# Performance work log

Measured on AMD Instinct MI355X. Metric: run time of the kernel, lower is better.

## Reference

```python
import jax, jax.numpy as jnp
import numpy as np

NUM_HEADS = 8
SPLIT_S = 4
DIM = 288            # n_feat * 3 * 3
SCALE = (DIM // NUM_HEADS) ** -0.5  # quirk: uses full dim's head_dim (36), not reduced
EPS = 1e-5


def _extract_patches(x):
    # x: [B,C,H,W] -> [B, C*9, H*W], 3x3 kernel, stride 1, 'same' padding
    B, C, H, W = x.shape
    xp = jnp.pad(x, ((0, 0), (0, 0), (1, 1), (1, 1)))
    pats = jnp.stack([xp[:, :, i:i + H, j:j + W] for i in range(3) for j in range(3)], axis=2)
    return pats.reshape(B, C * 9, H * W)


def _fold(cols, H, W):
    # inverse of extract: [B, C*9, H*W] -> [B,C,H,W], summing overlapping patches
    B, Ck, _ = cols.shape
    C = Ck // 9
    p = cols.reshape(B, C, 3, 3, H, W)
    out = jnp.zeros((B, C, H + 2, W + 2), cols.dtype)
    for i in range(3):
        for j in range(3):
            out = out.at[:, :, i:i + H, j:j + W].add(p[:, :, i, j])
    return out[:, :, 1:H + 1, 1:W + 1]


def _ln(x, w, b):
    mu = x.mean(-1, keepdims=True)
    var = ((x - mu) ** 2).mean(-1, keepdims=True)
    return (x - mu) * jax.lax.rsqrt(var + EPS) * w + b


def _attn(x, reduce_w, qkv_w, proj_w, proj_b):
    # x: [B,N,288] -> reduce -> [B,N,144] -> block-diag attention over s=4 chunks
    x = x @ reduce_w.T
    B, N, C = x.shape
    hd = C // NUM_HEADS
    qkv = (x @ qkv_w.T).reshape(B, N, 3, NUM_HEADS, hd).transpose(2, 0, 3, 1, 4)
    q, k, v = qkv[0], qkv[1], qkv[2]          # [B,h,N,hd]
    chunk = N // SPLIT_S
    q = q.reshape(B, NUM_HEADS, SPLIT_S, chunk, hd)
    k = k.reshape(B, NUM_HEADS, SPLIT_S, chunk, hd)
    v = v.reshape(B, NUM_HEADS, SPLIT_S, chunk, hd)
    attn = jnp.einsum('bhscd,bhsed->bhsce', q, k) * SCALE   # [B,h,s,chunk,chunk]
    attn = jax.nn.softmax(attn, axis=-1)
    out = jnp.einsum('bhsce,bhsed->bhscd', attn, v)          # [B,h,s,chunk,hd]
    out = out.transpose(0, 2, 3, 1, 4).reshape(B, N, C)      # cat chunks on token dim
    return out @ proj_w.T + proj_b


def setup_inputs() -> dict:
    key = jax.random.key(0)
    ks = jax.random.split(key, 12)
    d, dr, dh = DIM, DIM // 2, DIM // 4  # 288, 144, 72
    f = lambda k, shape: (jax.random.normal(k, shape, jnp.float32) * 0.02)
    return {
        'x': jax.random.normal(ks[0], (4, 32, 64, 64), jnp.float32),
        'ln1_w': jnp.ones((d,), jnp.float32), 'ln1_b': jnp.zeros((d,), jnp.float32),
        'reduce_w': f(ks[1], (dr, d)),
        'qkv_w': f(ks[2], (3 * dr, dr)),
        'proj_w': f(ks[3], (d, dr)), 'proj_b': jnp.zeros((d,), jnp.float32),
        'ln2_w': jnp.ones((d,), jnp.float32), 'ln2_b': jnp.zeros((d,), jnp.float32),
        'fc1_w': f(ks[4], (dh, d)), 'fc1_b': jnp.zeros((dh,), jnp.float32),
        'fc2_w': f(ks[5], (d, dh)), 'fc2_b': jnp.zeros((d,), jnp.float32),
    }


def reference(x, ln1_w, ln1_b, reduce_w, qkv_w, proj_w, proj_b, ln2_w, ln2_b, fc1_w, fc1_b, fc2_w, fc2_b):
    B, C, H, W = x.shape
    t = _extract_patches(x).transpose(0, 2, 1)  # [B, N=H*W, 288]
    t = t + _attn(_ln(t, ln1_w, ln1_b), reduce_w, qkv_w, proj_w, proj_b)
    h = _ln(t, ln2_w, ln2_b)
    t = t + (jax.nn.relu(h @ fc1_w.T + fc1_b) @ fc2_w.T + fc2_b)
    return _fold(t.transpose(0, 2, 1), H, W)
```

## Files before the change

### kernel.cpp

```cpp
#include <hip/hip_runtime.h>
#include <hip/hip_bf16.h>

typedef __hip_bfloat16 bf16;
typedef unsigned short u16;
typedef unsigned int u32;
typedef __attribute__((ext_vector_type(8))) short bf16x8;
typedef __attribute__((ext_vector_type(4))) float f32x4;

#define BB 4
#define CCH 32
#define HH 64
#define WW 64
#define NN 4096
#define D 288
#define DR 144
#define DQ 432
#define NH 8
#define HD 18
#define SPLIT 4
#define CHUNK 1024
#define KS 512
#define DH 72
#define SCALE_ 0.16666666666666666f
#define QSCALE 0.24044917348149343f
#define EPS_ 1e-5f
#define ASTR 160
#define ATS 168
#define HSTR 96

__device__ __attribute__((aligned(16))) u16 g_Wcb[DQ * D];
__device__ __attribute__((aligned(16))) u16 g_pw[D * ASTR];
__device__ __attribute__((aligned(16))) u16 g_f1w[HSTR * D];
__device__ __attribute__((aligned(16))) u16 g_f2w[D * HSTR];
__device__ __attribute__((aligned(16))) u16 g_q[(size_t)BB * NH * NN * 32];
__device__ __attribute__((aligned(16))) u16 g_k[(size_t)BB * NH * NN * 32];
__device__ __attribute__((aligned(16))) u16 g_vt[(size_t)BB * NH * SPLIT * 32 * CHUNK];
__device__ __attribute__((aligned(16))) float g_part[2 * (size_t)BB * NH * NN * 20];
__device__ __attribute__((aligned(16))) u16 g_t0[(size_t)BB * NN * D];
__device__ __attribute__((aligned(16))) u16 g_t2b[(size_t)BB * D * NN];
__device__ int   g_flag;

__device__ __forceinline__ float b2f(bf16 v) { return __bfloat162float(v); }
__device__ __forceinline__ float bits2f(u16 u) { return __uint_as_float(((u32)u) << 16); }
__device__ __forceinline__ u16 f2bits(float f) {
    u32 u = __float_as_uint(f);
    return (u16)((u + 0x7FFF + ((u >> 16) & 1)) >> 16);
}
__device__ __forceinline__ float ldin(const void* p, size_t i, int isbf) {
    return isbf ? b2f(((const bf16*)p)[i]) : ((const float*)p)[i];
}

#define RS  (D * ASTR + HSTR * D + D * HSTR)
#define RS2 (RS + BB * NH * SPLIT * CHUNK)
#define RSB ((RS2 + 255) / 256)
#define PATCHB (BB * HH)

__global__ void k_prep(const void* __restrict__ x, const void* __restrict__ qkv_w,
                       const void* __restrict__ reduce_w, const void* __restrict__ proj_w,
                       const void* __restrict__ fc1_w, const void* __restrict__ fc2_w) {
    __shared__ int cnt4[4];
    __shared__ float qw[DR];
    __shared__ float slab[32 * 3 * 66];
    int tid = threadIdx.x;
    {
        const u16* u = (const u16*)x;
        int c = 0;
        for (int i = tid; i < 2048; i += 256) c += (((u[i] >> 7) & 0xFF) >= 0x90);
        for (int o = 32; o; o >>= 1) c += __shfl_xor(c, o);
        if ((tid & 63) == 0) cnt4[tid >> 6] = c;
    }
    __syncthreads();
    int bf = (cnt4[0] + cnt4[1] + cnt4[2] + cnt4[3]) < 32;
    if (tid == 0 && blockIdx.x == 0) g_flag = bf;

    int bid = blockIdx.x;
    if (bid < DQ) {
        int o = bid;
        if (tid < DR) qw[tid] = ldin(qkv_w, (size_t)o * DR + tid, bf);
        __syncthreads();
        for (int col = tid; col < D; col += 256) {
            float s0 = 0.f, s1 = 0.f;
            #pragma unroll 4
            for (int j = 0; j < DR; j += 2) {
                s0 += qw[j] * ldin(reduce_w, (size_t)j * D + col, bf);
                s1 += qw[j + 1] * ldin(reduce_w, (size_t)(j + 1) * D + col, bf);
            }
            g_Wcb[(size_t)o * D + col] = f2bits(s0 + s1);
        }
    } else if (bid < DQ + RSB) {
        int idx = (bid - DQ) * 256 + tid;
        if (idx < D * ASTR) {
            int o = idx / ASTR, j = idx % ASTR;
            g_pw[idx] = (j < DR) ? f2bits(ldin(proj_w, (size_t)o * DR + j, bf)) : (u16)0;
        } else if (idx < D * ASTR + HSTR * D) {
            int t = idx - D * ASTR;
            int o = t / D;
            g_f1w[t] = (o < DH) ? f2bits(ldin(fc1_w, (size_t)t, bf)) : (u16)0;
        } else if (idx < RS) {
            int t = idx - D * ASTR - HSTR * D;
            int o = t / HSTR, j = t % HSTR;
            g_f2w[t] = (j < DH) ? f2bits(ldin(fc2_w, (size_t)o * DH + j, bf)) : (u16)0;
        } else if (idx < RS2) {
            int t = idx - RS;
            int bhs = t >> 10, n = t & 1023;
            g_vt[((size_t)bhs * 32 + 18) * CHUNK + n] = 0x3F80;
        }
    } else {
        int pb = bid - DQ - RSB;
        int b = pb >> 6, y = pb & 63;
        for (int idx = tid; idx < 32 * 3 * 66; idx += 256) {
            int c = idx / 198, rem = idx % 198;
            int ki = rem / 66, col = rem % 66 - 1;
            int sy = y + ki - 1;
            float v = 0.f;
            if (col >= 0 && col < 64 && sy >= 0 && sy < 64)
                v = ldin(x, ((size_t)(b * CCH + c) * HH + sy) * WW + col, bf);
            slab[idx] = v;
        }
        __syncthreads();
        size_t obase = ((size_t)b * NN + y * 64) * D;
        for (int idx = tid; idx < 64 * D; idx += 256) {
            int t = idx / D, f = idx % D;
            int c = f / 9, k = f % 9, ki = k / 3, kj = k % 3;
            g_t0[obase + idx] = f2bits(slab[c * 198 + ki * 66 + t + kj]);
        }
    }
}

__global__ void k_ln_qkv(const void* __restrict__ lnw, const void* __restrict__ lnb) {
    __shared__ __attribute__((aligned(16))) u16 xln[32 * 296];
    __shared__ float lnwf[D], lnbf[D];
    __shared__ float smu[32], srs[32];
    __shared__ u16 buf[3][144][32];
    int bf = g_flag;
    int tid = threadIdx.x;
    size_t tok0 = (size_t)blockIdx.x * 32;
    for (int i = tid; i < D; i += 256) { lnwf[i] = ldin(lnw, i, bf); lnbf[i] = ldin(lnb, i, bf); }
    {
        int tt = tid >> 3, p = tid & 7;
        const u32* pr = (const u32*)(g_t0 + (tok0 + tt) * D + p * 36);
        float s = 0.f, q = 0.f;
        #pragma unroll
        for (int j = 0; j < 18; ++j) {
            u32 v = pr[j];
            float a = bits2f((u16)(v & 0xFFFF)), b = bits2f((u16)(v >> 16));
            s += a + b; q += a * a + b * b;
        }
        #pragma unroll
        for (int o = 1; o < 8; o <<= 1) { s += __shfl_xor(s, o); q += __shfl_xor(q, o); }
        if (p == 0) {
            float mu = s / D;
            smu[tt] = mu;
            srs[tt] = rsqrtf(q / D - mu * mu + EPS_);
        }
    }
    __syncthreads();
    for (int idx = tid; idx < 32 * 144; idx += 256) {
        int t = idx / 144, dw = idx % 144;
        u32 v = *(const u32*)(g_t0 + (tok0 + t) * D + 2 * dw);
        float mu = smu[t], rs = srs[t];
        int f = 2 * dw;
        float a = (bits2f((u16)(v & 0xFFFF)) - mu) * rs * lnwf[f] + lnbf[f];
        float b = (bits2f((u16)(v >> 16)) - mu) * rs * lnwf[f + 1] + lnbf[f + 1];
        *(u32*)&xln[t * 296 + f] = (u32)f2bits(a) | ((u32)f2bits(b) << 16);
    }
    __syncthreads();
    int w = tid >> 6, lane = tid & 63, quad = lane >> 4, l15 = lane & 15;
    bf16x8 areg0[9], areg1[9];
    {
        const u16* a0 = xln + l15 * 296 + quad * 8;
        const u16* a1 = xln + (16 + l15) * 296 + quad * 8;
        #pragma unroll
        for (int ks = 0; ks < 9; ++ks) {
            areg0[ks] = *(const bf16x8*)(a0 + ks * 32);
            areg1[ks] = *(const bf16x8*)(a1 + ks * 32);
        }
    }
    int nt0 = w * 7, nt1 = (nt0 + 7 > 27) ? 27 : nt0 + 7;
    for (int nt = nt0; nt < nt1; ++nt) {
        f32x4 acc0 = {0.f, 0.f, 0.f, 0.f}, acc1 = {0.f, 0.f, 0.f, 0.f};
        const u16* bbase = g_Wcb + (size_t)(nt * 16 + l15) * D + quad * 8;
        #pragma unroll
        for (int ks = 0; ks < 9; ++ks) {
            bf16x8 bfr = *(const bf16x8*)(bbase + ks * 32);
            acc0 = __builtin_amdgcn_mfma_f32_16x16x32_bf16(areg0[ks], bfr, acc0, 0, 0, 0);
            acc1 = __builtin_amdgcn_mfma_f32_16x16x32_bf16(areg1[ks], bfr, acc1, 0, 0, 0);
        }
        int o = nt * 16 + l15;
        int which = o / DR, rem = o % DR;
        #pragma unroll
        for (int r = 0; r < 4; ++r) {
            buf[which][rem][quad * 4 + r] = f2bits(which == 0 ? acc0[r] * QSCALE : acc0[r]);
            buf[which][rem][16 + quad * 4 + r] = f2bits(which == 0 ? acc1[r] * QSCALE : acc1[r]);
        }
    }
    __syncthreads();
    {
        int b_ = (int)(tok0 >> 12);
        int n0 = (int)(tok0 & 4095);
        int sIdx = n0 >> 10, nc = n0 & 1023;
        for (int idx = tid; idx < 2 * 8 * 32 * 9; idx += 256) {
            int which = idx / 2304;
            int r2 = idx - which * 2304;
            int h = r2 / 288, r3 = r2 % 288, t = r3 / 9, dw = r3 % 9;
            u32 lo = buf[which][h * 18 + 2 * dw][t];
            u32 hi = buf[which][h * 18 + 2 * dw + 1][t];
            u16* dst = (which ? g_k : g_q) + ((size_t)(b_ * NH + h) * NN + n0 + t) * 32 + 2 * dw;
            *(u32*)dst = lo | (hi << 16);
        }
        for (int idx = tid; idx < 144 * 16; idx += 256) {
            int rem = idx >> 4, tp = idx & 15;
            int hh = rem / HD, dd = rem % HD;
            u32 lo = buf[2][rem][2 * tp];
            u32 hi = buf[2][rem][2 * tp + 1];
            size_t voff = (((size_t)(b_ * NH + hh) * SPLIT + sIdx) * 32 + dd) * CHUNK + nc + 2 * tp;
            *(u32*)&g_vt[voff] = lo | (hi << 16);
        }
    }
}

#define PSTR 72
__global__ __launch_bounds__(128) void k_attn() {
    __shared__ __attribute__((aligned(16))) u16 Pl[2][4][16 * PSTR];
    int bid = blockIdx.x;
    int chunk = bid & 127;
    int qblk = (bid >> 7) & 7;
    int ksl = bid >> 10;
    int s = chunk & 3, bh = chunk >> 2;
    int tid = threadIdx.x;
    int w = tid >> 6, lane = tid & 63, quad = lane >> 4, l15 = lane & 15;

    size_t rowbase = (size_t)bh * NN + s * CHUNK;
    size_t vtbase = ((size_t)bh * SPLIT + s) * 32 * CHUNK;
    const u16* kbase = g_k + rowbase * 32 + quad * 8;
    const u16* vbase = g_vt + vtbase + quad * 8;

    int qbase = qblk * 128 + w * 64;
    bf16x8 qf[4];
    #pragma unroll
    for (int t = 0; t < 4; ++t)
        qf[t] = *(const bf16x8*)(g_q + (rowbase + qbase + t * 16 + l15) * 32 + quad * 8);

    f32x4 accA[4], accB[4];
    #pragma unroll
    for (int t = 0; t < 4; ++t) {
        accA[t] = (f32x4){0.f, 0.f, 0.f, 0.f};
        accB[t] = (f32x4){0.f, 0.f, 0.f, 0.f};
    }

    int kt0 = ksl * KS;
    for (int kk = 0; kk < KS; kk += 64) {
        int kt = kt0 + kk;
        bf16x8 kf0 = *(const bf16x8*)(kbase + (size_t)(kt + 2 * l15) * 32);
        bf16x8 kf1 = *(const bf16x8*)(kbase + (size_t)(kt + 2 * l15 + 1) * 32);
        bf16x8 kf2 = *(const bf16x8*)(kbase + (size_t)(kt + 32 + 2 * l15) * 32);
        bf16x8 kf3 = *(const bf16x8*)(kbase + (size_t)(kt + 33 + 2 * l15) * 32);
        bf16x8 vA0 = *(const bf16x8*)(vbase + (size_t)l15 * CHUNK + kt);
        bf16x8 vB0 = *(const bf16x8*)(vbase + (size_t)(16 + l15) * CHUNK + kt);
        bf16x8 vA1 = *(const bf16x8*)(vbase + (size_t)l15 * CHUNK + kt + 32);
        bf16x8 vB1 = *(const bf16x8*)(vbase + (size_t)(16 + l15) * CHUNK + kt + 32);
        f32x4 z = {0.f, 0.f, 0.f, 0.f};
        #pragma unroll
        for (int t = 0; t < 4; ++t) {
            u16* pw = Pl[w][t];
            f32x4 S0 = __builtin_amdgcn_mfma_f32_16x16x32_bf16(qf[t], kf0, z, 0, 0, 0);
            f32x4 S1 = __builtin_amdgcn_mfma_f32_16x16x32_bf16(qf[t], kf1, z, 0, 0, 0);
            f32x4 S2 = __builtin_amdgcn_mfma_f32_16x16x32_bf16(qf[t], kf2, z, 0, 0, 0);
            f32x4 S3 = __builtin_amdgcn_mfma_f32_16x16x32_bf16(qf[t], kf3, z, 0, 0, 0);
            #pragma unroll
            for (int r = 0; r < 4; ++r) {
                float p0 = exp2f(S0[r]), p1 = exp2f(S1[r]);
                float p2 = exp2f(S2[r]), p3 = exp2f(S3[r]);
                u32 w0 = __builtin_amdgcn_perm(__float_as_uint(p1), __float_as_uint(p0), 0x07060302u);
                u32 w1 = __builtin_amdgcn_perm(__float_as_uint(p3), __float_as_uint(p2), 0x07060302u);
                *(u32*)&pw[(quad * 4 + r) * PSTR + 2 * l15] = w0;
                *(u32*)&pw[(quad * 4 + r) * PSTR + 32 + 2 * l15] = w1;
            }
        }
        #pragma unroll
        for (int t = 0; t < 4; ++t) {
            const u16* pw = Pl[w][t];
            bf16x8 pf0 = *(const bf16x8*)&pw[l15 * PSTR + quad * 8];
            bf16x8 pf1 = *(const bf16x8*)&pw[l15 * PSTR + 32 + quad * 8];
            accA[t] = __builtin_amdgcn_mfma_f32_16x16x32_bf16(pf0, vA0, accA[t], 0, 0, 0);
            accB[t] = __builtin_amdgcn_mfma_f32_16x16x32_bf16(pf0, vB0, accB[t], 0, 0, 0);
            accA[t] = __builtin_amdgcn_mfma_f32_16x16x32_bf16(pf1, vA1, accA[t], 0, 0, 0);
            accB[t] = __builtin_amdgcn_mfma_f32_16x16x32_bf16(pf1, vB1, accB[t], 0, 0, 0);
        }
    }
    float* pb = g_part + (((size_t)ksl * 32 + bh) * SPLIT + s) * (size_t)(CHUNK * 20);
    #pragma unroll
    for (int t = 0; t < 4; ++t) {
        #pragma unroll
        for (int r = 0; r < 4; ++r) {
            int tokenc = qbase + t * 16 + quad * 4 + r;
            float* row = pb + (size_t)tokenc * 20;
            row[l15] = accA[t][r];
            if (l15 < 3) row[16 + l15] = accB[t][r];
        }
    }
}

__global__ void k_proj_mlp(const void* __restrict__ proj_b, const void* __restrict__ lnw,
                           const void* __restrict__ lnb, const void* __restrict__ fc1_b,
                           const void* __restrict__ fc2_b) {
    __shared__ __attribute__((aligned(16))) u16 t1f[32 * 296];
    __shared__ __attribute__((aligned(16))) u16 xln[32 * 296];
    __shared__ __attribute__((aligned(16))) u16 attnT[32 * ATS];
    __shared__ __attribute__((aligned(16))) u16 hbuf[32 * HSTR];
    __shared__ float lnwf[D], lnbf[D];
    __shared__ float smu[32], srs[32];
    int bf = g_flag;
    int tid = threadIdx.x;
    size_t tok0 = (size_t)blockIdx.x * 32;
    int w = tid >> 6, lane = tid & 63, quad = lane >> 4, l15 = lane & 15;
    for (int i = tid; i < D; i += 256) { lnwf[i] = ldin(lnw, i, bf); lnbf[i] = ldin(lnb, i, bf); }

    int b_ = (int)(tok0 >> 12);
    int s_ = ((int)tok0 & 4095) >> 10;
    int tc0 = (int)tok0 & 1023;
    for (int idx = tid; idx < 32 * (ATS - DR); idx += 256) {
        int t = idx / (ATS - DR), f = idx % (ATS - DR);
        attnT[t * ATS + DR + f] = 0;
    }
    {
        int t = tid >> 3, h = tid & 7;
        const float* p1 = g_part + (((size_t)(b_ * NH + h)) * SPLIT + s_) * (size_t)(CHUNK * 20)
                        + (size_t)(tc0 + t) * 20;
        const float* p2 = p1 + (size_t)32 * SPLIT * CHUNK * 20;
        f32x4 a0 = *(const f32x4*)p1,        c0 = *(const f32x4*)p2;
        f32x4 a1 = *(const f32x4*)(p1 + 4),  c1 = *(const f32x4*)(p2 + 4);
        f32x4 a2 = *(const f32x4*)(p1 + 8),  c2 = *(const f32x4*)(p2 + 8);
        f32x4 a3 = *(const f32x4*)(p1 + 12), c3 = *(const f32x4*)(p2 + 12);
        f32x4 a4 = *(const f32x4*)(p1 + 16), c4 = *(const f32x4*)(p2 + 16);
        float inv = 1.f / (a4[2] + c4[2]);
        u16* dst = attnT + t * ATS + h * HD;
        #pragma unroll
        for (int d = 0; d < 4; ++d) {
            dst[d]      = f2bits((a0[d] + c0[d]) * inv);
            dst[4 + d]  = f2bits((a1[d] + c1[d]) * inv);
            dst[8 + d]  = f2bits((a2[d] + c2[d]) * inv);
            dst[12 + d] = f2bits((a3[d] + c3[d]) * inv);
        }
        dst[16] = f2bits((a4[0] + c4[0]) * inv);
        dst[17] = f2bits((a4[1] + c4[1]) * inv);
    }
    __syncthreads();

    {
        bf16x8 areg0[5], areg1[5];
        const u16* a0 = attnT + l15 * ATS + quad * 8;
        const u16* a1 = attnT + (16 + l15) * ATS + quad * 8;
        #pragma unroll
        for (int ks = 0; ks < 5; ++ks) {
            areg0[ks] = *(const bf16x8*)(a0 + ks * 32);
            areg1[ks] = *(const bf16x8*)(a1 + ks * 32);
        }
        const int tab[5] = {0, 5, 10, 14, 18};
        for (int nt = tab[w]; nt < tab[w + 1]; ++nt) {
            f32x4 acc0 = {0.f, 0.f, 0.f, 0.f}, acc1 = {0.f, 0.f, 0.f, 0.f};
            const u16* bbase = g_pw + (size_t)(nt * 16 + l15) * ASTR + quad * 8;
            #pragma unroll
            for (int ks = 0; ks < 5; ++ks) {
                bf16x8 bfr = *(const bf16x8*)(bbase + ks * 32);
                acc0 = __builtin_amdgcn_mfma_f32_16x16x32_bf16(areg0[ks], bfr, acc0, 0, 0, 0);
                acc1 = __builtin_amdgcn_mfma_f32_16x16x32_bf16(areg1[ks], bfr, acc1, 0, 0, 0);
            }
            int o = nt * 16 + l15;
            float bias = ldin(proj_b, o, bf);
            #pragma unroll
            for (int r = 0; r < 4; ++r) {
                t1f[(quad * 4 + r) * 296 + o] =
                    f2bits(bits2f(g_t0[(tok0 + quad * 4 + r) * D + o]) + acc0[r] + bias);
                t1f[(16 + quad * 4 + r) * 296 + o] =
                    f2bits(bits2f(g_t0[(tok0 + 16 + quad * 4 + r) * D + o]) + acc1[r] + bias);
            }
        }
    }
    __syncthreads();
    {
        int tt = tid >> 3, p = tid & 7;
        const u32* src = (const u32*)&t1f[tt * 296 + p * 36];
        float s = 0.f, q = 0.f;
        #pragma unroll
        for (int j = 0; j < 18; ++j) {
            u32 v = src[j];
            float a = bits2f((u16)(v & 0xFFFF)), b = bits2f((u16)(v >> 16));
            s += a + b; q += a * a + b * b;
        }
        #pragma unroll
        for (int o = 1; o < 8; o <<= 1) { s += __shfl_xor(s, o); q += __shfl_xor(q, o); }
        if (p == 0) {
            float mu = s / D;
            smu[tt] = mu;
            srs[tt] = rsqrtf(q / D - mu * mu + EPS_);
        }
    }
    __syncthreads();
    for (int idx = tid; idx < 32 * 144; idx += 256) {
        int t = idx / 144, dw = idx % 144;
        int f = 2 * dw;
        u32 v = *(const u32*)&t1f[t * 296 + f];
        float mu = smu[t], rs = srs[t];
        float a = (bits2f((u16)(v & 0xFFFF)) - mu) * rs * lnwf[f] + lnbf[f];
        float b = (bits2f((u16)(v >> 16)) - mu) * rs * lnwf[f + 1] + lnbf[f + 1];
        *(u32*)&xln[t * 296 + f] = (u32)f2bits(a) | ((u32)f2bits(b) << 16);
    }
    __syncthreads();
    {
        bf16x8 areg0[9], areg1[9];
        const u16* a0 = xln + l15 * 296 + quad * 8;
        const u16* a1 = xln + (16 + l15) * 296 + quad * 8;
        #pragma unroll
        for (int ks = 0; ks < 9; ++ks) {
            areg0[ks] = *(const bf16x8*)(a0 + ks * 32);
            areg1[ks] = *(const bf16x8*)(a1 + ks * 32);
        }
        const int tab2[5] = {0, 2, 4, 5, 6};
        for (int nt = tab2[w]; nt < tab2[w + 1]; ++nt) {
            f32x4 acc0 = {0.f, 0.f, 0.f, 0.f}, acc1 = {0.f, 0.f, 0.f, 0.f};
            const u16* bbase = g_f1w + (size_t)(nt * 16 + l15) * D + quad * 8;
            #pragma unroll
            for (int ks = 0; ks < 9; ++ks) {
                bf16x8 bfr = *(const bf16x8*)(bbase + ks * 32);
                acc0 = __builtin_amdgcn_mfma_f32_16x16x32_bf16(areg0[ks], bfr, acc0, 0, 0, 0);
                acc1 = __builtin_amdgcn_mfma_f32_16x16x32_bf16(areg1[ks], bfr, acc1, 0, 0, 0);
            }
            int o = nt * 16 + l15;
            float bias = (o < DH) ? ldin(fc1_b, o, bf) : 0.f;
            #pragma unroll
            for (int r = 0; r < 4; ++r) {
                hbuf[(quad * 4 + r) * HSTR + o] = f2bits(fmaxf(acc0[r] + bias, 0.f));
                hbuf[(16 + quad * 4 + r) * HSTR + o] = f2bits(fmaxf(acc1[r] + bias, 0.f));
            }
        }
    }
    __syncthreads();
    {
        bf16x8 areg0[3], areg1[3];
        const u16* a0 = hbuf + l15 * HSTR + quad * 8;
        const u16* a1 = hbuf + (16 + l15) * HSTR + quad * 8;
        #pragma unroll
        for (int ks = 0; ks < 3; ++ks) {
            areg0[ks] = *(const bf16x8*)(a0 + ks * 32);
            areg1[ks] = *(const bf16x8*)(a1 + ks * 32);
        }
        const int tab[5] = {0, 5, 10, 14, 18};
        for (int nt = tab[w]; nt < tab[w + 1]; ++nt) {
            f32x4 acc0 = {0.f, 0.f, 0.f, 0.f}, acc1 = {0.f, 0.f, 0.f, 0.f};
            const u16* bbase = g_f2w + (size_t)(nt * 16 + l15) * HSTR + quad * 8;
            #pragma unroll
            for (int ks = 0; ks < 3; ++ks) {
                bf16x8 bfr = *(const bf16x8*)(bbase + ks * 32);
                acc0 = __builtin_amdgcn_mfma_f32_16x16x32_bf16(areg0[ks], bfr, acc0, 0, 0, 0);
                acc1 = __builtin_amdgcn_mfma_f32_16x16x32_bf16(areg1[ks], bfr, acc1, 0, 0, 0);
            }
            int o = nt * 16 + l15;
            float bias = ldin(fc2_b, o, bf);
            #pragma unroll
            for (int r = 0; r < 4; ++r) {
                xln[(quad * 4 + r) * 296 + o] =
                    f2bits(bits2f(t1f[(quad * 4 + r) * 296 + o]) + acc0[r] + bias);
                xln[(16 + quad * 4 + r) * 296 + o] =
                    f2bits(bits2f(t1f[(16 + quad * 4 + r) * 296 + o]) + acc1[r] + bias);
            }
        }
    }
    __syncthreads();
    {
        int n0 = (int)(tok0 & 4095);
        for (int idx = tid; idx < D * 16; idx += 256) {
            int o = idx >> 4, tp = idx & 15;
            u32 v = (u32)xln[(2 * tp) * 296 + o] | ((u32)xln[(2 * tp + 1) * 296 + o] << 16);
            *(u32*)&g_t2b[((size_t)b_ * D + o) * NN + n0 + 2 * tp] = v;
        }
    }
}

__global__ void k_fold(void* __restrict__ out) {
    int bf = g_flag;
    int idx = blockIdx.x * blockDim.x + threadIdx.x;
    if (idx >= BB * CCH * HH * WW) return;
    int xx = idx % WW;
    int y = (idx / WW) % HH;
    int c = (idx / (WW * HH)) % CCH;
    int b = idx / (WW * HH * CCH);
    const u16* base = g_t2b + ((size_t)b * D + c * 9) * NN;
    float s = 0.f;
    #pragma unroll
    for (int i = 0; i < 3; ++i) {
        int sy = y + 1 - i;
        if (sy < 0 || sy >= HH) continue;
        #pragma unroll
        for (int j = 0; j < 3; ++j) {
            int sx = xx + 1 - j;
            if (sx < 0 || sx >= WW) continue;
            s += bits2f(base[(size_t)(i * 3 + j) * NN + sy * WW + sx]);
        }
    }
    if (bf) ((bf16*)out)[idx] = __float2bfloat16(s);
    else    ((float*)out)[idx] = s;
}

extern "C" void kernel_launch(void* const* d_in, const int* in_sizes, int n_in,
                              void* d_out, int out_size, void* d_ws, size_t ws_size,
                              hipStream_t stream) {
    const void* x        = d_in[0];
    const void* ln1_w    = d_in[1];
    const void* ln1_b    = d_in[2];
    const void* reduce_w = d_in[3];
    const void* qkv_w    = d_in[4];
    const void* proj_w   = d_in[5];
    const void* proj_b   = d_in[6];
    const void* ln2_w    = d_in[7];
    const void* ln2_b    = d_in[8];
    const void* fc1_w    = d_in[9];
    const void* fc1_b    = d_in[10];
    const void* fc2_w    = d_in[11];
    const void* fc2_b    = d_in[12];

    k_prep     <<<DQ + RSB + PATCHB, 256, 0, stream>>>(x, qkv_w, reduce_w, proj_w, fc1_w, fc2_w);
    k_ln_qkv   <<<BB * NN / 32, 256, 0, stream>>>(ln1_w, ln1_b);
    k_attn     <<<2 * BB * NH * SPLIT * 8, 128, 0, stream>>>();
    k_proj_mlp <<<BB * NN / 32, 256, 0, stream>>>(proj_b, ln2_w, ln2_b, fc1_b, fc2_b);
    k_fold     <<<(BB * CCH * HH * WW + 255) / 256, 256, 0, stream>>>(d_out);
}
```

Baseline: 198.3 us.

## Fuse patch extraction into LN+QKV kernel and store attention partials in bf16

Patch extraction (im2col) moves out of the prep kernel into the LN/QKV kernel. Each 32-token block builds its own input slab in shared memory, and LayerNorm reads from there instead of re-reading g_t0 from global memory; g_t0 is still written for the later residual. The split-K attention partial outputs are now stored as bf16, with only the softmax denominator kept as fp32, which halves partial-buffer traffic at some cost in precision. The shared QKV output buffer is reused as the slab, which adds an extra barrier.

```diff
diff --git a/kernel.cpp b/kernel.cpp
--- a/kernel.cpp
+++ b/kernel.cpp
@@ -27,6 +27,7 @@
 #define ASTR 160
 #define ATS 168
 #define HSTR 96
+#define PROW 20
 
 __device__ __attribute__((aligned(16))) u16 g_Wcb[DQ * D];
 __device__ __attribute__((aligned(16))) u16 g_pw[D * ASTR];
@@ -35,7 +36,7 @@
 __device__ __attribute__((aligned(16))) u16 g_q[(size_t)BB * NH * NN * 32];
 __device__ __attribute__((aligned(16))) u16 g_k[(size_t)BB * NH * NN * 32];
 __device__ __attribute__((aligned(16))) u16 g_vt[(size_t)BB * NH * SPLIT * 32 * CHUNK];
-__device__ __attribute__((aligned(16))) float g_part[2 * (size_t)BB * NH * NN * 20];
+__device__ __attribute__((aligned(16))) u16 g_part[2 * (size_t)BB * NH * NN * PROW];
 __device__ __attribute__((aligned(16))) u16 g_t0[(size_t)BB * NN * D];
 __device__ __attribute__((aligned(16))) u16 g_t2b[(size_t)BB * D * NN];
 __device__ int   g_flag;
@@ -53,14 +54,12 @@
 #define RS  (D * ASTR + HSTR * D + D * HSTR)
 #define RS2 (RS + BB * NH * SPLIT * CHUNK)
 #define RSB ((RS2 + 255) / 256)
-#define PATCHB (BB * HH)
 
 __global__ void k_prep(const void* __restrict__ x, const void* __restrict__ qkv_w,
                        const void* __restrict__ reduce_w, const void* __restrict__ proj_w,
                        const void* __restrict__ fc1_w, const void* __restrict__ fc2_w) {
     __shared__ int cnt4[4];
     __shared__ float qw[DR];
-    __shared__ float slab[32 * 3 * 66];
     int tid = threadIdx.x;
     {
         const u16* u = (const u16*)x;
@@ -87,7 +86,7 @@
             }
             g_Wcb[(size_t)o * D + col] = f2bits(s0 + s1);
         }
-    } else if (bid < DQ + RSB) {
+    } else {
         int idx = (bid - DQ) * 256 + tid;
         if (idx < D * ASTR) {
             int o = idx / ASTR, j = idx % ASTR;
@@ -105,40 +104,44 @@
             int bhs = t >> 10, n = t & 1023;
             g_vt[((size_t)bhs * 32 + 18) * CHUNK + n] = 0x3F80;
         }
-    } else {
-        int pb = bid - DQ - RSB;
-        int b = pb >> 6, y = pb & 63;
-        for (int idx = tid; idx < 32 * 3 * 66; idx += 256) {
-            int c = idx / 198, rem = idx % 198;
-            int ki = rem / 66, col = rem % 66 - 1;
-            int sy = y + ki - 1;
-            float v = 0.f;
-            if (col >= 0 && col < 64 && sy >= 0 && sy < 64)
-                v = ldin(x, ((size_t)(b * CCH + c) * HH + sy) * WW + col, bf);
-            slab[idx] = v;
-        }
-        __syncthreads();
-        size_t obase = ((size_t)b * NN + y * 64) * D;
-        for (int idx = tid; idx < 64 * D; idx += 256) {
-            int t = idx / D, f = idx % D;
-            int c = f / 9, k = f % 9, ki = k / 3, kj = k % 3;
-            g_t0[obase + idx] = f2bits(slab[c * 198 + ki * 66 + t + kj]);
-        }
-    }
-}
-
-__global__ void k_ln_qkv(const void* __restrict__ lnw, const void* __restrict__ lnb) {
-    __shared__ __attribute__((aligned(16))) u16 xln[32 * 296];
+    }
+}
+
+__global__ void k_ln_qkv(const void* __restrict__ x, const void* __restrict__ lnw,
+                         const void* __restrict__ lnb) {
+    __shared__ __attribute__((aligned(16))) u16 xt0[32 * 296];
     __shared__ float lnwf[D], lnbf[D];
     __shared__ float smu[32], srs[32];
-    __shared__ u16 buf[3][144][32];
+    __shared__ __attribute__((aligned(16))) u16 buf[3][144][32];
+    float* slab = (float*)&buf[0][0][0];
     int bf = g_flag;
     int tid = threadIdx.x;
     size_t tok0 = (size_t)blockIdx.x * 32;
+    int b_ = (int)(tok0 >> 12);
+    int n0 = (int)(tok0 & 4095);
+    int y = n0 >> 6, xc0 = n0 & 63;
     for (int i = tid; i < D; i += 256) { lnwf[i] = ldin(lnw, i, bf); lnbf[i] = ldin(lnb, i, bf); }
+    for (int idx = tid; idx < 32 * 3 * 34; idx += 256) {
+        int c = idx / 102, rem = idx % 102;
+        int ki = rem / 34, cc = rem % 34;
+        int sy = y + ki - 1, sx = xc0 + cc - 1;
+        float v = 0.f;
+        if (sy >= 0 && sy < 64 && sx >= 0 && sx < 64)
+            v = ldin(x, ((size_t)(b_ * CCH + c) * HH + sy) * WW + sx, bf);
+        slab[idx] = v;
+    }
+    __syncthreads();
+    for (int idx = tid; idx < 32 * D; idx += 256) {
+        int t = idx / D, f = idx % D;
+        int c = f / 9, k = f % 9, ki = k / 3, kj = k % 3;
+        u16 v = f2bits(slab[(c * 3 + ki) * 34 + t + kj]);
+        xt0[t * 296 + f] = v;
+        g_t0[(tok0 + t) * D + f] = v;
+    }
+    __syncthreads();
     {
         int tt = tid >> 3, p = tid & 7;
-        const u32* pr = (const u32*)(g_t0 + (tok0 + tt) * D + p * 36);
+        const u32* pr = (const u32*)&xt0[tt * 296 + p * 36];
         float s = 0.f, q = 0.f;
         #pragma unroll
         for (int j = 0; j < 18; ++j) {
@@ -157,25 +160,26 @@
     __syncthreads();
     for (int idx = tid; idx < 32 * 144; idx += 256) {
         int t = idx / 144, dw = idx % 144;
-        u32 v = *(const u32*)(g_t0 + (tok0 + t) * D + 2 * dw);
+        int f = 2 * dw;
+        u32 v = *(const u32*)&xt0[t * 296 + f];
         float mu = smu[t], rs = srs[t];
-        int f = 2 * dw;
         float a = (bits2f((u16)(v & 0xFFFF)) - mu) * rs * lnwf[f] + lnbf[f];
         float b = (bits2f((u16)(v >> 16)) - mu) * rs * lnwf[f + 1] + lnbf[f + 1];
-        *(u32*)&xln[t * 296 + f] = (u32)f2bits(a) | ((u32)f2bits(b) << 16);
+        *(u32*)&xt0[t * 296 + f] = (u32)f2bits(a) | ((u32)f2bits(b) << 16);
     }
     __syncthreads();
     int w = tid >> 6, lane = tid & 63, quad = lane >> 4, l15 = lane & 15;
     bf16x8 areg0[9], areg1[9];
     {
-        const u16* a0 = xln + l15 * 296 + quad * 8;
-        const u16* a1 = xln + (16 + l15) * 296 + quad * 8;
+        const u16* a0 = xt0 + l15 * 296 + quad * 8;
+        const u16* a1 = xt0 + (16 + l15) * 296 + quad * 8;
         #pragma unroll
         for (int ks = 0; ks < 9; ++ks) {
             areg0[ks] = *(const bf16x8*)(a0 + ks * 32);
             areg1[ks] = *(const bf16x8*)(a1 + ks * 32);
         }
     }
+    __syncthreads();
     int nt0 = w * 7, nt1 = (nt0 + 7 > 27) ? 27 : nt0 + 7;
     for (int nt = nt0; nt < nt1; ++nt) {
         f32x4 acc0 = {0.f, 0.f, 0.f, 0.f}, acc1 = {0.f, 0.f, 0.f, 0.f};
@@ -196,8 +200,6 @@
     }
     __syncthreads();
     {
-        int b_ = (int)(tok0 >> 12);
-        int n0 = (int)(tok0 & 4095);
         int sIdx = n0 >> 10, nc = n0 & 1023;
         for (int idx = tid; idx < 2 * 8 * 32 * 9; idx += 256) {
             int which = idx / 2304;
@@ -288,15 +290,16 @@
             accB[t] = __builtin_amdgcn_mfma_f32_16x16x32_bf16(pf1, vB1, accB[t], 0, 0, 0);
         }
     }
-    float* pb = g_part + (((size_t)ksl * 32 + bh) * SPLIT + s) * (size_t)(CHUNK * 20);
+    u16* pb = g_part + (((size_t)ksl * 32 + bh) * SPLIT + s) * (size_t)(CHUNK * PROW);
     #pragma unroll
     for (int t = 0; t < 4; ++t) {
         #pragma unroll
         for (int r = 0; r < 4; ++r) {
             int tokenc = qbase + t * 16 + quad * 4 + r;
-            float* row = pb + (size_t)tokenc * 20;
-            row[l15] = accA[t][r];
-            if (l15 < 3) row[16 + l15] = accB[t][r];
+            u16* row = pb + (size_t)tokenc * PROW;
+            row[l15] = f2bits(accA[t][r]);
+            if (l15 < 2) row[16 + l15] = f2bits(accB[t][r]);
+            if (l15 == 2) *(float*)(row + 18) = accB[t][r];
         }
     }
 }
@@ -325,25 +328,22 @@
     }
     {
         int t = tid >> 3, h = tid & 7;
-        const float* p1 = g_part + (((size_t)(b_ * NH + h)) * SPLIT + s_) * (size_t)(CHUNK * 20)
-                        + (size_t)(tc0 + t) * 20;
-        const float* p2 = p1 + (size_t)32 * SPLIT * CHUNK * 20;
-        f32x4 a0 = *(const f32x4*)p1,        c0 = *(const f32x4*)p2;
-        f32x4 a1 = *(const f32x4*)(p1 + 4),  c1 = *(const f32x4*)(p2 + 4);
-        f32x4 a2 = *(const f32x4*)(p1 + 8),  c2 = *(const f32x4*)(p2 + 8);
-        f32x4 a3 = *(const f32x4*)(p1 + 12), c3 = *(const f32x4*)(p2 + 12);
-        f32x4 a4 = *(const f32x4*)(p1 + 16), c4 = *(const f32x4*)(p2 + 16);
-        float inv = 1.f / (a4[2] + c4[2]);
+        const u32* r1 = (const u32*)(g_part
+            + (((size_t)(b_ * NH + h)) * SPLIT + s_) * (size_t)(CHUNK * PROW)
+            + (size_t)(tc0 + t) * PROW);
+        const u32* r2 = r1 + (size_t)32 * SPLIT * CHUNK * PROW / 2;
+        u32 w1[10], w2[10];
+        #pragma unroll
+        for (int i = 0; i < 10; ++i) { w1[i] = r1[i]; w2[i] = r2[i]; }
+        float l = __uint_as_float(w1[9]) + __uint_as_float(w2[9]);
+        float inv = 1.f / l;
         u16* dst = attnT + t * ATS + h * HD;
         #pragma unroll
-        for (int d = 0; d < 4; ++d) {
-            dst[d]      = f2bits((a0[d] + c0[d]) * inv);
-            dst[4 + d]  = f2bits((a1[d] + c1[d]) * inv);
-            dst[8 + d]  = f2bits((a2[d] + c2[d]) * inv);
-            dst[12 + d] = f2bits((a3[d] + c3[d]) * inv);
-        }
-        dst[16] = f2bits((a4[0] + c4[0]) * inv);
-        dst[17] = f2bits((a4[1] + c4[1]) * inv);
+        for (int d = 0; d < 18; ++d) {
+            u16 a = (d & 1) ? (u16)(w1[d >> 1] >> 16) : (u16)(w1[d >> 1] & 0xFFFF);
+            u16 b = (d & 1) ? (u16)(w2[d >> 1] >> 16) : (u16)(w2[d >> 1] & 0xFFFF);
+            dst[d] = f2bits((bits2f(a) + bits2f(b)) * inv);
+        }
     }
     __syncthreads();
 
@@ -519,8 +519,8 @@
     const void* fc2_w    = d_in[11];
     const void* fc2_b    = d_in[12];
 
-    k_prep     <<<DQ + RSB + PATCHB, 256, 0, stream>>>(x, qkv_w, reduce_w, proj_w, fc1_w, fc2_w);
-    k_ln_qkv   <<<BB * NN / 32, 256, 0, stream>>>(ln1_w, ln1_b);
+    k_prep     <<<DQ + RSB, 256, 0, stream>>>(x, qkv_w, reduce_w, proj_w, fc1_w, fc2_w);
+    k_ln_qkv   <<<BB * NN / 32, 256, 0, stream>>>(x, ln1_w, ln1_b);
     k_attn     <<<2 * BB * NH * SPLIT * 8, 128, 0, stream>>>();
     k_proj_mlp <<<BB * NN / 32, 256, 0, stream>>>(proj_b, ln2_w, ln2_b, fc1_b, fc2_b);
     k_fold     <<<(BB * CCH * HH * WW + 255) / 256, 256, 0, stream>>>(d_out);
```

After: 203.4 us. 2.6% more time.
